# Kernel tuning notes

Hardware: AMD Instinct MI355X
Metric: run time of the kernel (lower is better)

The kernel has to match this reference:

```python
import jax, jax.numpy as jnp
import numpy as np
from jax import lax

FILTERS = 8      # Conv1D filters per column
K = 5            # kernel_size
ACTION_DIM = 2
COLS = [16, 128, 1024]  # columns entering each of the 3 blocks (grow x FILTERS)


def setup_inputs() -> dict:
    key = jax.random.key(0)
    ks = jax.random.split(key, 8)
    B, L, C = 64, 128, 16
    state = jax.random.normal(ks[0], (B, L, C), jnp.float32)
    inp = {"state": state}
    # One grouped-conv kernel per block: WIO layout [K, in_per_group=1, cols*FILTERS].
    # Channel c*FILTERS+f of the output is column c's filter f (matches Keras concat order).
    for i, c in enumerate(COLS):
        inp[f"k{i+1}"] = jax.random.normal(ks[1 + i], (K, 1, c * FILTERS), jnp.float32) * 0.1
        inp[f"b{i+1}"] = jnp.zeros((c * FILTERS,), jnp.float32)
    L_final = L - len(COLS) * (K - 1)          # 116
    feat = L_final * COLS[-1] * FILTERS        # 950272
    inp["W"] = jax.random.normal(ks[4], (feat, ACTION_DIM), jnp.float32) * 1e-3
    inp["bd"] = jnp.zeros((ACTION_DIM,), jnp.float32)
    return inp


def _block(x, kern, bias):
    # x: [B, cols, L]  ->  [B, cols*FILTERS, L-K+1]
    cols = x.shape[1]
    xin = jnp.transpose(x, (0, 2, 1))  # [B, L, cols] (NWC)
    y = lax.conv_general_dilated(
        xin, kern, window_strides=(1,), padding='VALID',
        dimension_numbers=('NWC', 'WIO', 'NWC'), feature_group_count=cols)
    y = jax.nn.relu(y + bias)          # [B, L', cols*FILTERS]
    return jnp.transpose(y, (0, 2, 1))


def reference(state, k1, b1, k2, b2, k3, b3, W, bd):
    # Actor.call: transpose [B,L,C] -> [B,C,L], run blocks, transpose back, flatten, dense+tanh
    x = jnp.transpose(state, (0, 2, 1))  # [B, cols=16, L=128]
    for kern, bias in ((k1, b1), (k2, b2), (k3, b3)):
        x = _block(x, kern, bias)
    x = jnp.transpose(x, (0, 2, 1)).reshape(state.shape[0], -1)  # [B, L'*channels]
    return jnp.tanh(x @ W + bd)  # [B, ACTION_DIM]
```

## Files before the change

kernel.cpp:

```cpp
#include <hip/hip_runtime.h>
#include <math.h>

#define NB    64
#define L0    128
#define C0    16
#define KW    5
#define NF    8
#define L1    124
#define L2    120
#define L3    116
#define CH1   128
#define CH2   1024
#define CH3   8192
#define NCHUNK 8
#define NS     4
#define SLICE  29
#define TROWS  (SLICE + 4)
#define Y1R    (SLICE + 8)
#define STR    (SLICE + 12)
#define NFH    4

__global__ __launch_bounds__(256, 8) void actor_fused_kernel(
    const float* __restrict__ state,
    const float* __restrict__ k1,
    const float* __restrict__ b1,
    const float* __restrict__ k2,
    const float* __restrict__ b2,
    const float* __restrict__ k3,
    const float* __restrict__ b3,
    const float* __restrict__ W,
    float* __restrict__ partials)
{
    const int chunk = blockIdx.x;
    const int b     = blockIdx.y;
    const int slice = blockIdx.z;
    const int t0    = slice * SLICE;
    const int tid   = threadIdx.x;
    const int c3loc = tid >> 1;
    const int fh    = tid & 1;
    const int c3    = chunk * 128 + c3loc;

    __shared__ float s_state[STR][2];
    __shared__ float s_y1[Y1R][16];
    __shared__ float tile[TROWS][128];

    if (tid < STR * 2) {
        int r = tid >> 1, c = tid & 1;
        s_state[r][c] = state[(size_t)b * L0 * C0 + (t0 + r) * C0 + chunk * 2 + c];
    }
    __syncthreads();

    for (int idx = tid; idx < Y1R * 16; idx += 256) {
        int r = idx >> 4, jloc = idx & 15;
        int j = chunk * 16 + jloc;
        int cloc = jloc >> 3;
        float acc = b1[j];
#pragma unroll
        for (int k = 0; k < KW; ++k)
            acc = fmaf(s_state[r + k][cloc], k1[k * CH1 + j], acc);
        s_y1[r][jloc] = fmaxf(acc, 0.f);
    }
    __syncthreads();

    {
        int c = tid & 127, h = tid >> 7;
        int m = chunk * 128 + c;
        int jloc = c >> 3;
        float kk[KW], bb = b2[m];
#pragma unroll
        for (int k = 0; k < KW; ++k) kk[k] = k2[k * CH2 + m];
        int r0 = h ? 17 : 0, r1 = h ? TROWS : 17;
        for (int r = r0; r < r1; ++r) {
            float acc = bb;
#pragma unroll
            for (int k = 0; k < KW; ++k)
                acc = fmaf(s_y1[r + k][jloc], kk[k], acc);
            tile[r][c] = fmaxf(acc, 0.f);
        }
    }

    float kw[KW][NFH], bv[NFH];
#pragma unroll
    for (int k = 0; k < KW; ++k)
#pragma unroll
        for (int f = 0; f < NFH; ++f)
            kw[k][f] = k3[k * CH3 + c3 * NF + fh * NFH + f];
#pragma unroll
    for (int f = 0; f < NFH; ++f)
        bv[f] = b3[c3 * NF + fh * NFH + f];

    __syncthreads();

    float a0x = 0.f, a0y = 0.f, a1x = 0.f, a1y = 0.f;

    const float4* __restrict__ wp =
        (const float4*)W + (size_t)t0 * 4096 + (size_t)c3 * 4 + fh * 2;

    float w0 = tile[0][c3loc];
    float w1 = tile[1][c3loc];
    float w2 = tile[2][c3loc];
    float w3 = tile[3][c3loc];

    for (int t = 0; t < SLICE; ++t) {
        float w4 = tile[t + 4][c3loc];

        float v[NFH];
#pragma unroll
        for (int f = 0; f < NFH; ++f) {
            float a = bv[f];
            a = fmaf(w0, kw[0][f], a);
            a = fmaf(w1, kw[1][f], a);
            a = fmaf(w2, kw[2][f], a);
            a = fmaf(w3, kw[3][f], a);
            a = fmaf(w4, kw[4][f], a);
            v[f] = fmaxf(a, 0.f);
        }

        float4 q0 = wp[0];
        float4 q1 = wp[1];
        wp += 4096;

        a0x = fmaf(v[0], q0.x, a0x); a0y = fmaf(v[0], q0.y, a0y);
        a0x = fmaf(v[1], q0.z, a0x); a0y = fmaf(v[1], q0.w, a0y);
        a1x = fmaf(v[2], q1.x, a1x); a1y = fmaf(v[2], q1.y, a1y);
        a1x = fmaf(v[3], q1.z, a1x); a1y = fmaf(v[3], q1.w, a1y);

        w0 = w1; w1 = w2; w2 = w3; w3 = w4;
    }

    float acc0 = a0x + a1x;
    float acc1 = a0y + a1y;

#pragma unroll
    for (int d = 32; d >= 1; d >>= 1) {
        acc0 += __shfl_down(acc0, d, 64);
        acc1 += __shfl_down(acc1, d, 64);
    }
    __shared__ float red[4][2];
    int wave = tid >> 6, lane = tid & 63;
    if (lane == 0) { red[wave][0] = acc0; red[wave][1] = acc1; }
    __syncthreads();
    if (tid == 0) {
        size_t o = (((size_t)b * NCHUNK + chunk) * NS + slice) * 2;
        partials[o + 0] = (red[0][0] + red[1][0]) + (red[2][0] + red[3][0]);
        partials[o + 1] = (red[0][1] + red[1][1]) + (red[2][1] + red[3][1]);
    }
}

__global__ __launch_bounds__(128) void finish_kernel(
    const float* __restrict__ partials,
    const float* __restrict__ bd,
    float* __restrict__ out)
{
    int i = threadIdx.x;
    int b = i >> 1, a = i & 1;
    float s = bd[a];
#pragma unroll
    for (int p = 0; p < NCHUNK * NS; ++p)
        s += partials[((size_t)b * NCHUNK * NS + p) * 2 + a];
    out[b * 2 + a] = tanhf(s);
}

extern "C" void kernel_launch(void* const* d_in, const int* in_sizes, int n_in,
                              void* d_out, int out_size, void* d_ws, size_t ws_size,
                              hipStream_t stream) {
    const float* state = (const float*)d_in[0];
    const float* k1    = (const float*)d_in[1];
    const float* b1    = (const float*)d_in[2];
    const float* k2    = (const float*)d_in[3];
    const float* b2    = (const float*)d_in[4];
    const float* k3    = (const float*)d_in[5];
    const float* b3    = (const float*)d_in[6];
    const float* W     = (const float*)d_in[7];
    const float* bd    = (const float*)d_in[8];
    float* out = (float*)d_out;

    float* partials = (float*)d_ws;

    dim3 grid(NCHUNK, NB, NS);
    actor_fused_kernel<<<grid, 256, 0, stream>>>(
        state, k1, b1, k2, b2, k3, b3, W, partials);

    finish_kernel<<<1, 128, 0, stream>>>(partials, bd, out);
}
```

Before: 98.38 us.

## Process four batch elements per block to reuse dense weight loads

Each block now handles four batch samples instead of one, computing the conv stages for all four into shared memory. Each dense-layer weight float4 loaded from global memory is then reused across the four samples. This is meant to cut the repeated streaming of the large W matrix, which was reread once per batch element. In exchange the grid shrinks fourfold, shared memory and register use grow, and the launch-bounds occupancy hint is lowered.

```diff
diff --git a/kernel.cpp b/kernel.cpp
--- a/kernel.cpp
+++ b/kernel.cpp
@@ -19,8 +19,10 @@
 #define Y1R    (SLICE + 8)
 #define STR    (SLICE + 12)
 #define NFH    4
-
-__global__ __launch_bounds__(256, 8) void actor_fused_kernel(
+#define NBATCH 4
+#define NBG    (NB / NBATCH)
+
+__global__ __launch_bounds__(256, 2) void actor_fused_kernel(
     const float* __restrict__ state,
     const float* __restrict__ k1,
     const float* __restrict__ b1,
@@ -32,7 +34,7 @@
     float* __restrict__ partials)
 {
     const int chunk = blockIdx.x;
-    const int b     = blockIdx.y;
+    const int bg    = blockIdx.y;
     const int slice = blockIdx.z;
     const int t0    = slice * SLICE;
     const int tid   = threadIdx.x;
@@ -40,25 +42,33 @@
     const int fh    = tid & 1;
     const int c3    = chunk * 128 + c3loc;
 
-    __shared__ float s_state[STR][2];
-    __shared__ float s_y1[Y1R][16];
-    __shared__ float tile[TROWS][128];
-
-    if (tid < STR * 2) {
-        int r = tid >> 1, c = tid & 1;
-        s_state[r][c] = state[(size_t)b * L0 * C0 + (t0 + r) * C0 + chunk * 2 + c];
-    }
-    __syncthreads();
-
-    for (int idx = tid; idx < Y1R * 16; idx += 256) {
-        int r = idx >> 4, jloc = idx & 15;
-        int j = chunk * 16 + jloc;
-        int cloc = jloc >> 3;
-        float acc = b1[j];
-#pragma unroll
-        for (int k = 0; k < KW; ++k)
-            acc = fmaf(s_state[r + k][cloc], k1[k * CH1 + j], acc);
-        s_y1[r][jloc] = fmaxf(acc, 0.f);
+    __shared__ float s_state[NBATCH][STR][2];
+    __shared__ float s_y1[NBATCH][Y1R][16];
+    __shared__ float tile[NBATCH][TROWS][128];
+
+    {
+        int bb = tid >> 6, lt = tid & 63;
+        const float* sp = state + (size_t)(bg * NBATCH + bb) * L0 * C0
+                        + (size_t)t0 * C0 + chunk * 2;
+        for (int i = lt; i < STR * 2; i += 64) {
+            int r = i >> 1, c = i & 1;
+            s_state[bb][r][c] = sp[r * C0 + c];
+        }
+    }
+    __syncthreads();
+
+    {
+        int bb = tid >> 6, lt = tid & 63;
+        for (int i = lt; i < Y1R * 16; i += 64) {
+            int r = i >> 4, jloc = i & 15;
+            int j = chunk * 16 + jloc;
+            int cloc = jloc >> 3;
+            float acc = b1[j];
+#pragma unroll
+            for (int k = 0; k < KW; ++k)
+                acc = fmaf(s_state[bb][r + k][cloc], k1[k * CH1 + j], acc);
+            s_y1[bb][r][jloc] = fmaxf(acc, 0.f);
+        }
     }
     __syncthreads();
 
@@ -66,17 +76,19 @@
         int c = tid & 127, h = tid >> 7;
         int m = chunk * 128 + c;
         int jloc = c >> 3;
-        float kk[KW], bb = b2[m];
+        float kk[KW], b2v = b2[m];
 #pragma unroll
         for (int k = 0; k < KW; ++k) kk[k] = k2[k * CH2 + m];
         int r0 = h ? 17 : 0, r1 = h ? TROWS : 17;
-        for (int r = r0; r < r1; ++r) {
-            float acc = bb;
-#pragma unroll
-            for (int k = 0; k < KW; ++k)
-                acc = fmaf(s_y1[r + k][jloc], kk[k], acc);
-            tile[r][c] = fmaxf(acc, 0.f);
-        }
+#pragma unroll
+        for (int bb = 0; bb < NBATCH; ++bb)
+            for (int r = r0; r < r1; ++r) {
+                float acc = b2v;
+#pragma unroll
+                for (int k = 0; k < KW; ++k)
+                    acc = fmaf(s_y1[bb][r + k][jloc], kk[k], acc);
+                tile[bb][r][c] = fmaxf(acc, 0.f);
+            }
     }
 
     float kw[KW][NFH], bv[NFH];
@@ -91,59 +103,75 @@
 
     __syncthreads();
 
-    float a0x = 0.f, a0y = 0.f, a1x = 0.f, a1y = 0.f;
+    float ax[NBATCH], ay[NBATCH];
+#pragma unroll
+    for (int bb = 0; bb < NBATCH; ++bb) { ax[bb] = 0.f; ay[bb] = 0.f; }
+
+    float w[NBATCH][4];
+#pragma unroll
+    for (int bb = 0; bb < NBATCH; ++bb)
+#pragma unroll
+        for (int r = 0; r < 4; ++r)
+            w[bb][r] = tile[bb][r][c3loc];
 
     const float4* __restrict__ wp =
         (const float4*)W + (size_t)t0 * 4096 + (size_t)c3 * 4 + fh * 2;
 
-    float w0 = tile[0][c3loc];
-    float w1 = tile[1][c3loc];
-    float w2 = tile[2][c3loc];
-    float w3 = tile[3][c3loc];
-
     for (int t = 0; t < SLICE; ++t) {
-        float w4 = tile[t + 4][c3loc];
-
-        float v[NFH];
-#pragma unroll
-        for (int f = 0; f < NFH; ++f) {
-            float a = bv[f];
-            a = fmaf(w0, kw[0][f], a);
-            a = fmaf(w1, kw[1][f], a);
-            a = fmaf(w2, kw[2][f], a);
-            a = fmaf(w3, kw[3][f], a);
-            a = fmaf(w4, kw[4][f], a);
-            v[f] = fmaxf(a, 0.f);
-        }
-
         float4 q0 = wp[0];
         float4 q1 = wp[1];
         wp += 4096;
 
-        a0x = fmaf(v[0], q0.x, a0x); a0y = fmaf(v[0], q0.y, a0y);
-        a0x = fmaf(v[1], q0.z, a0x); a0y = fmaf(v[1], q0.w, a0y);
-        a1x = fmaf(v[2], q1.x, a1x); a1y = fmaf(v[2], q1.y, a1y);
-        a1x = fmaf(v[3], q1.z, a1x); a1y = fmaf(v[3], q1.w, a1y);
-
-        w0 = w1; w1 = w2; w2 = w3; w3 = w4;
-    }
-
-    float acc0 = a0x + a1x;
-    float acc1 = a0y + a1y;
-
-#pragma unroll
-    for (int d = 32; d >= 1; d >>= 1) {
-        acc0 += __shfl_down(acc0, d, 64);
-        acc1 += __shfl_down(acc1, d, 64);
-    }
-    __shared__ float red[4][2];
+        float v[NBATCH][NFH];
+#pragma unroll
+        for (int bb = 0; bb < NBATCH; ++bb) {
+            float w4 = tile[bb][t + 4][c3loc];
+#pragma unroll
+            for (int f = 0; f < NFH; ++f) {
+                float a = bv[f];
+                a = fmaf(w[bb][0], kw[0][f], a);
+                a = fmaf(w[bb][1], kw[1][f], a);
+                a = fmaf(w[bb][2], kw[2][f], a);
+                a = fmaf(w[bb][3], kw[3][f], a);
+                a = fmaf(w4,       kw[4][f], a);
+                v[bb][f] = fmaxf(a, 0.f);
+            }
+            w[bb][0] = w[bb][1]; w[bb][1] = w[bb][2];
+            w[bb][2] = w[bb][3]; w[bb][3] = w4;
+        }
+
+#pragma unroll
+        for (int bb = 0; bb < NBATCH; ++bb) {
+            ax[bb] = fmaf(v[bb][0], q0.x, ax[bb]); ay[bb] = fmaf(v[bb][0], q0.y, ay[bb]);
+            ax[bb] = fmaf(v[bb][1], q0.z, ax[bb]); ay[bb] = fmaf(v[bb][1], q0.w, ay[bb]);
+            ax[bb] = fmaf(v[bb][2], q1.x, ax[bb]); ay[bb] = fmaf(v[bb][2], q1.y, ay[bb]);
+            ax[bb] = fmaf(v[bb][3], q1.z, ax[bb]); ay[bb] = fmaf(v[bb][3], q1.w, ay[bb]);
+        }
+    }
+
+#pragma unroll
+    for (int bb = 0; bb < NBATCH; ++bb) {
+#pragma unroll
+        for (int d = 32; d >= 1; d >>= 1) {
+            ax[bb] += __shfl_down(ax[bb], d, 64);
+            ay[bb] += __shfl_down(ay[bb], d, 64);
+        }
+    }
+    __shared__ float red[4][NBATCH][2];
     int wave = tid >> 6, lane = tid & 63;
-    if (lane == 0) { red[wave][0] = acc0; red[wave][1] = acc1; }
-    __syncthreads();
-    if (tid == 0) {
-        size_t o = (((size_t)b * NCHUNK + chunk) * NS + slice) * 2;
-        partials[o + 0] = (red[0][0] + red[1][0]) + (red[2][0] + red[3][0]);
-        partials[o + 1] = (red[0][1] + red[1][1]) + (red[2][1] + red[3][1]);
+    if (lane == 0) {
+#pragma unroll
+        for (int bb = 0; bb < NBATCH; ++bb) {
+            red[wave][bb][0] = ax[bb];
+            red[wave][bb][1] = ay[bb];
+        }
+    }
+    __syncthreads();
+    if (tid < NBATCH * 2) {
+        int bb = tid >> 1, a = tid & 1;
+        float s = (red[0][bb][a] + red[1][bb][a]) + (red[2][bb][a] + red[3][bb][a]);
+        int b = bg * NBATCH + bb;
+        partials[(((size_t)b * NCHUNK + chunk) * NS + slice) * 2 + a] = s;
     }
 }
 
@@ -177,7 +205,7 @@
 
     float* partials = (float*)d_ws;
 
-    dim3 grid(NCHUNK, NB, NS);
+    dim3 grid(NCHUNK, NBG, NS);
     actor_fused_kernel<<<grid, 256, 0, stream>>>(
         state, k1, b1, k2, b2, k3, b3, W, partials);
 
```

After: 93.06 us. -5.4%, faster.
